# Optimization experiments

Hardware: AMD Instinct MI355X
Metric: run time of the kernel (lower is better)

Reference implementation:

```python
import jax, jax.numpy as jnp
import numpy as np

SEQ = 4096
EMBED = 1280
HEADS = 16
HEAD_DIM = EMBED // HEADS  # 80


def rotate_half(x):
    # interleaved rotate: out[..., 2i] = -x[..., 2i+1]; out[..., 2i+1] = x[..., 2i]
    x_even = x[..., ::2]
    x_odd = x[..., 1::2]
    return jnp.stack((-x_odd, x_even), axis=-1).reshape(x.shape)


def setup_inputs() -> dict:
    key = jax.random.key(0)
    ks = jax.random.split(key, 7)
    return {
        "hidden_states": jax.random.normal(ks[0], (SEQ, EMBED), dtype=jnp.float32),
        "cos": jax.random.uniform(ks[1], (SEQ, HEAD_DIM), dtype=jnp.float32),
        "sin": jax.random.uniform(ks[2], (SEQ, HEAD_DIM), dtype=jnp.float32),
        "w_qkv": jax.random.normal(ks[3], (EMBED, 3 * EMBED), dtype=jnp.float32) * 0.02,
        "b_qkv": jax.random.normal(ks[4], (3 * EMBED,), dtype=jnp.float32) * 0.02,
        "w_proj": jax.random.normal(ks[5], (EMBED, EMBED), dtype=jnp.float32) * 0.02,
        "b_proj": jax.random.normal(ks[6], (EMBED,), dtype=jnp.float32) * 0.02,
    }


def reference(hidden_states, cos, sin, w_qkv, b_qkv, w_proj, b_proj):
    S = hidden_states.shape[0]
    # QKV projection: (S, 3E) -> (S, 3, H, D)
    qkv = (hidden_states @ w_qkv + b_qkv).reshape(S, 3, HEADS, HEAD_DIM)
    q, k, v = qkv[:, 0], qkv[:, 1], qkv[:, 2]  # each (S, H, D)

    # RoPE in float32, cos/sin broadcast over heads: (S, 1, D)
    dt = q.dtype
    qf, kf = q.astype(jnp.float32), k.astype(jnp.float32)
    c = cos[:, None, :].astype(jnp.float32)
    s = sin[:, None, :].astype(jnp.float32)
    q = (qf * c + rotate_half(qf) * s).astype(dt)
    k = (kf * c + rotate_half(kf) * s).astype(dt)

    scaling = HEAD_DIM ** -0.5
    # attention scores per head: (H, S, S)
    scores = jnp.einsum("shd,thd->hst", q, k) * scaling
    attn = jax.nn.softmax(scores.astype(jnp.float32), axis=-1).astype(dt)
    # weighted values: (S, H, D)
    out = jnp.einsum("hst,thd->shd", attn, v).reshape(S, EMBED)
    return out @ w_proj + b_proj
```

## Files before the change

### kernel.cpp

```cpp
#include <hip/hip_runtime.h>
#include <hip/hip_bf16.h>

#define SEQ   4096
#define EMBED 1280
#define NH    16
#define HD    80
#define K1    EMBED
#define N1    (3*EMBED)

typedef short bfrag_t __attribute__((ext_vector_type(8)));
typedef float f32x4   __attribute__((ext_vector_type(4)));
typedef float f32x16  __attribute__((ext_vector_type(16)));

static __device__ __forceinline__ unsigned short f2bf(float x){
    __hip_bfloat16 h = __float2bfloat16(x);
    return __builtin_bit_cast(unsigned short, h);
}
static __device__ __forceinline__ float bf2f(unsigned short u){
    unsigned int v = ((unsigned int)u) << 16;
    return __builtin_bit_cast(float, v);
}

static __device__ __forceinline__ unsigned int pack2bf(float a, float b){
    unsigned int ua = __builtin_bit_cast(unsigned int, a) + 0x8000u;
    unsigned int ub = __builtin_bit_cast(unsigned int, b) + 0x8000u;
#if __has_builtin(__builtin_amdgcn_perm)
    return __builtin_amdgcn_perm(ub, ua, 0x07060302u);
#else
    return (ua >> 16) | (ub & 0xFFFF0000u);
#endif
}

static __device__ __forceinline__ float fast_exp2(float x){
#if __has_builtin(__builtin_amdgcn_exp2f)
    return __builtin_amdgcn_exp2f(x);
#else
    return __expf(x * 0.69314718056f);
#endif
}

static __device__ __forceinline__ void gload_lds16(const void* g, void* l){
#if __has_builtin(__builtin_amdgcn_global_load_lds)
    __builtin_amdgcn_global_load_lds(
        (const __attribute__((address_space(1))) unsigned int*)g,
        (__attribute__((address_space(3))) unsigned int*)l, 16, 0, 0);
#else
    *(uint4*)l = *(const uint4*)g;
#endif
}

static __device__ __forceinline__ bfrag_t ld_frag8(const unsigned short* p){
    uint2 lo = *(const uint2*)p;
    uint2 hi = *(const uint2*)(p + 4);
    uint4 u; u.x = lo.x; u.y = lo.y; u.z = hi.x; u.w = hi.y;
    return __builtin_bit_cast(bfrag_t, u);
}


__global__ __launch_bounds__(256) void f32_to_bf16_k(const float* __restrict__ in,
                                                     unsigned short* __restrict__ out){
    int i = blockIdx.x * 256 + threadIdx.x;
    float4 v = ((const float4*)in)[i];
    ushort4 r;
    r.x = f2bf(v.x); r.y = f2bf(v.y); r.z = f2bf(v.z); r.w = f2bf(v.w);
    ((ushort4*)out)[i] = r;
}

__global__ __launch_bounds__(256) void transpose_to_bf16(const float* __restrict__ in,
                                                         unsigned short* __restrict__ out,
                                                         int R, int C){
    __shared__ float t[32][33];
    int bc = blockIdx.x * 32, br = blockIdx.y * 32;
    int tx = threadIdx.x & 31, ty = threadIdx.x >> 5;
    for (int i = ty; i < 32; i += 8) t[i][tx] = in[(size_t)(br + i) * C + bc + tx];
    __syncthreads();
    for (int i = ty; i < 32; i += 8) out[(size_t)(bc + i) * R + br + tx] = f2bf(t[tx][i]);
}


__global__ __launch_bounds__(256)
void gemm_qkv(const unsigned short* __restrict__ A,
              const unsigned short* __restrict__ BT,
              const float* __restrict__ bias,
              const float* __restrict__ cosp, const float* __restrict__ sinp,
              unsigned short* __restrict__ qout, unsigned short* __restrict__ kout,
              unsigned short* __restrict__ vout,
              int M, int N, int K)
{
    __shared__ union {
        struct { unsigned short A[128*32]; unsigned short B[128*32]; } ab;
        unsigned short tr[4][64][72];
    } lds;

    int tid  = threadIdx.x;
    int lane = tid & 63, wave = tid >> 6;
    int wm = wave >> 1, wn = wave & 1;
    int quad = lane >> 4, l16 = lane & 15;
    int m0 = blockIdx.y * 128, n0 = blockIdx.x * 128;

    f32x4 acc[4][4] = {};
    const unsigned short* ga = A  + (size_t)(m0 + (tid>>2)) * K + (tid&3)*8;
    const unsigned short* gb = BT + (size_t)(n0 + (tid>>2)) * K + (tid&3)*8;

    for (int k0 = 0; k0 < K; k0 += 32){
        __syncthreads();
        gload_lds16(ga,                &lds.ab.A[tid*8]);
        gload_lds16(ga + (size_t)64*K, &lds.ab.A[2048 + tid*8]);
        gload_lds16(gb,                &lds.ab.B[tid*8]);
        gload_lds16(gb + (size_t)64*K, &lds.ab.B[2048 + tid*8]);
        ga += 32; gb += 32;
        __syncthreads();
        bfrag_t af[4], bf[4];
        #pragma unroll
        for (int i = 0; i < 4; i++)
            af[i] = *(const bfrag_t*)&lds.ab.A[(wm*64 + i*16 + l16)*32 + quad*8];
        #pragma unroll
        for (int j = 0; j < 4; j++)
            bf[j] = *(const bfrag_t*)&lds.ab.B[(wn*64 + j*16 + l16)*32 + quad*8];
        #pragma unroll
        for (int i = 0; i < 4; i++)
            #pragma unroll
            for (int j = 0; j < 4; j++)
                acc[i][j] = __builtin_amdgcn_mfma_f32_16x16x32_bf16(af[i], bf[j], acc[i][j], 0, 0, 0);
    }

    const float scaling = 0.11180339887498949f;

    if (n0 >= 2*EMBED){
        __syncthreads();
        #pragma unroll
        for (int j = 0; j < 4; j++){
            int colw = j*16 + l16;
            float b = bias[n0 + wn*64 + colw];
            #pragma unroll
            for (int i = 0; i < 4; i++){
                ushort4 u;
                u.x = f2bf(acc[i][j][0] + b);
                u.y = f2bf(acc[i][j][1] + b);
                u.z = f2bf(acc[i][j][2] + b);
                u.w = f2bf(acc[i][j][3] + b);
                *(ushort4*)&lds.tr[wave][colw][i*16 + quad*4] = u;
            }
        }
        int c8 = lane >> 3, rc = lane & 7;
        #pragma unroll
        for (int cg = 0; cg < 8; cg++){
            int colw = cg*8 + c8;
            size_t colg = (size_t)(n0 - 2*EMBED) + wn*64 + colw;
            int rowg = m0 + wm*64 + rc*8;
            *(uint4*)&vout[colg*SEQ + rowg] = *(const uint4*)&lds.tr[wave][colw][rc*8];
        }
        return;
    }

    #pragma unroll
    for (int i = 0; i < 4; i++)
    #pragma unroll
    for (int j = 0; j < 4; j++){
        int col = n0 + wn*64 + j*16 + l16;
        float b = bias[col];
        #pragma unroll
        for (int r = 0; r < 4; r++){
            int row = m0 + wm*64 + i*16 + quad*4 + r;
            float v = acc[i][j][r] + b;
            int which = col / EMBED;
            int rem   = col % EMBED;
            int h = rem / HD, d = rem % HD;
            float vo = __shfl_xor(v, 1, 64);
            float c = cosp[(size_t)row*HD + d];
            float s = sinp[(size_t)row*HD + d];
            float o = (d & 1) ? (v*c + vo*s) : (v*c - vo*s);
            if (which == 0)
                qout[((size_t)h*SEQ + row)*HD + d] = f2bf(o * scaling);
            else
                kout[((size_t)h*SEQ + row)*HD + d] = f2bf(o);
        }
    }
}


__global__ __launch_bounds__(256)
void gemm_proj(const unsigned short* __restrict__ A,
               const unsigned short* __restrict__ BT,
               const float* __restrict__ bias,
               float* __restrict__ out,
               int M, int N, int K)
{
    __shared__ unsigned short As[64*32];
    __shared__ unsigned short Bs[128*32];
    int tid  = threadIdx.x;
    int lane = tid & 63, wave = tid >> 6;
    int wm = wave & 1, wn = wave >> 1;
    int quad = lane >> 4, l16 = lane & 15;
    int m0 = blockIdx.y * 64, n0 = blockIdx.x * 128;

    f32x4 acc[2][4] = {};
    const unsigned short* ga = A  + (size_t)(m0 + (tid>>2)) * K + (tid&3)*8;
    const unsigned short* gb = BT + (size_t)(n0 + (tid>>2)) * K + (tid&3)*8;

    for (int k0 = 0; k0 < K; k0 += 32){
        __syncthreads();
        gload_lds16(ga,                &As[tid*8]);
        gload_lds16(gb,                &Bs[tid*8]);
        gload_lds16(gb + (size_t)64*K, &Bs[2048 + tid*8]);
        ga += 32; gb += 32;
        __syncthreads();
        bfrag_t af[2], bf[4];
        #pragma unroll
        for (int i = 0; i < 2; i++)
            af[i] = *(const bfrag_t*)&As[(wm*32 + i*16 + l16)*32 + quad*8];
        #pragma unroll
        for (int j = 0; j < 4; j++)
            bf[j] = *(const bfrag_t*)&Bs[(wn*64 + j*16 + l16)*32 + quad*8];
        #pragma unroll
        for (int i = 0; i < 2; i++)
            #pragma unroll
            for (int j = 0; j < 4; j++)
                acc[i][j] = __builtin_amdgcn_mfma_f32_16x16x32_bf16(af[i], bf[j], acc[i][j], 0, 0, 0);
    }

    #pragma unroll
    for (int i = 0; i < 2; i++)
    #pragma unroll
    for (int j = 0; j < 4; j++){
        int col = n0 + wn*64 + j*16 + l16;
        float b = bias[col];
        #pragma unroll
        for (int r = 0; r < 4; r++){
            int row = m0 + wm*32 + i*16 + quad*4 + r;
            out[(size_t)row * N + col] = acc[i][j][r] + b;
        }
    }
}


__global__ __launch_bounds__(256, 4)
void attn_mfma(const unsigned short* __restrict__ q,
               const unsigned short* __restrict__ k,
               const unsigned short* __restrict__ vt,
               unsigned short* __restrict__ out,
               unsigned short* __restrict__ opart,
               float* __restrict__ lpart,
               int iters)
{
    __shared__ unsigned short Vt[2][80*64];
    __shared__ unsigned short Ps[128][68];

    int tid  = threadIdx.x;
    int lane = tid & 63, wave = tid >> 6;
    int quad = lane >> 4, l16 = lane & 15;
    int l32  = lane & 31, h2 = lane >> 5;
    int h = blockIdx.y, q0 = blockIdx.x * 128;
    int split = blockIdx.z;
    int kb0 = split * iters * 64;
    int qrow = wave*32 + l32;

    const unsigned short* qh = q  + ((size_t)h*SEQ + q0)*HD;
    const unsigned short* kh = k  + (size_t)h*SEQ*HD;
    const unsigned short* vh = vt + (size_t)h*HD*SEQ;

    bfrag_t qf[5];
    #pragma unroll
    for (int kk = 0; kk < 5; kk++)
        qf[kk] = *(const bfrag_t*)&qh[(size_t)qrow*HD + (kk*2 + h2)*8];

    auto stage = [&](int buf, int kb){
        unsigned short* dst = &Vt[buf][0];
        #pragma unroll
        for (int rnd = 0; rnd < 3; rnd++){
            int idx = rnd*256 + tid;
            if (rnd < 2 || tid < 128){
                int row = idx >> 3, c = idx & 7;
                gload_lds16(&vh[(size_t)row*SEQ + kb + ((c ^ (row & 7)) << 3)], &dst[idx*8]);
            }
        }
    };

    stage(0, kb0);

    float la = 0.f, lb = 0.f;
    f32x4 o_[2][5] = {};

    const unsigned short* kp = kh + (size_t)(kb0 + l32)*HD + h2*8;
    const float LOG2E = 1.44269504f;
    const float BIAS2 = -17.3123405f;

    for (int kt = 0; kt < iters; kt++){
        f32x16 S0 = {}, S1 = {};
        #pragma unroll
        for (int kk = 0; kk < 5; kk++){
            bfrag_t kf0 = *(const bfrag_t*)(kp + kk*16);
            bfrag_t kf1 = *(const bfrag_t*)(kp + (size_t)32*HD + kk*16);
            S0 = __builtin_amdgcn_mfma_f32_32x32x16_bf16(kf0, qf[kk], S0, 0,0,0);
            S1 = __builtin_amdgcn_mfma_f32_32x32x16_bf16(kf1, qf[kk], S1, 0,0,0);
        }
        kp += (size_t)64*HD;

        #pragma unroll
        for (int r = 0; r < 16; r++){
            float p0 = fast_exp2(fmaf(S0[r], LOG2E, BIAS2));
            float p1 = fast_exp2(fmaf(S1[r], LOG2E, BIAS2));
            S0[r] = p0; S1[r] = p1;
            la += p0; lb += p1;
        }

        #pragma unroll
        for (int g = 0; g < 4; g++){
            uint2 w0, w1;
            w0.x = pack2bf(S0[g*4+0], S0[g*4+1]);
            w0.y = pack2bf(S0[g*4+2], S0[g*4+3]);
            w1.x = pack2bf(S1[g*4+0], S1[g*4+1]);
            w1.y = pack2bf(S1[g*4+2], S1[g*4+3]);
            *(uint2*)&Ps[qrow][g*8 + h2*4]      = w0;
            *(uint2*)&Ps[qrow][32 + g*8 + h2*4] = w1;
        }

        __syncthreads();
        if (kt + 1 < iters) stage((kt+1)&1, kb0 + (kt+1)*64);

        int buf = kt & 1;
        #pragma unroll
        for (int kk = 0; kk < 2; kk++){
            bfrag_t pf0 = ld_frag8(&Ps[wave*32      + l16][kk*32 + quad*8]);
            bfrag_t pf1 = ld_frag8(&Ps[wave*32 + 16 + l16][kk*32 + quad*8]);
            #pragma unroll
            for (int dt = 0; dt < 5; dt++){
                int row = dt*16 + l16;
                bfrag_t vf = *(const bfrag_t*)&Vt[buf][row*64 + (((kk*4+quad) ^ (l16 & 7)) << 3)];
                o_[0][dt] = __builtin_amdgcn_mfma_f32_16x16x32_bf16(vf, pf0, o_[0][dt], 0,0,0);
                o_[1][dt] = __builtin_amdgcn_mfma_f32_16x16x32_bf16(vf, pf1, o_[1][dt], 0,0,0);
            }
        }
    }

    float l_ = la + lb;
    l_ += __shfl_xor(l_, 32, 64);

    if (gridDim.z == 1){
        #pragma unroll
        for (int i = 0; i < 2; i++){
            float linv = 1.f / __shfl(l_, i*16 + l16, 64);
            int qg = q0 + wave*32 + i*16 + l16;
            #pragma unroll
            for (int dt = 0; dt < 5; dt++){
                int d = dt*16 + quad*4;
                ushort4 u;
                u.x = f2bf(o_[i][dt][0]*linv);
                u.y = f2bf(o_[i][dt][1]*linv);
                u.z = f2bf(o_[i][dt][2]*linv);
                u.w = f2bf(o_[i][dt][3]*linv);
                *(ushort4*)&out[(size_t)qg*EMBED + h*HD + d] = u;
            }
        }
    } else {
        if (h2 == 0)
            lpart[((size_t)(split*NH + h))*SEQ + q0 + qrow] = l_;
        #pragma unroll
        for (int i = 0; i < 2; i++){
            int qg = q0 + wave*32 + i*16 + l16;
            size_t base = (((size_t)(split*NH + h))*SEQ + qg)*HD;
            #pragma unroll
            for (int dt = 0; dt < 5; dt++){
                int d = dt*16 + quad*4;
                ushort4 u;
                u.x = f2bf(o_[i][dt][0]);
                u.y = f2bf(o_[i][dt][1]);
                u.z = f2bf(o_[i][dt][2]);
                u.w = f2bf(o_[i][dt][3]);
                *(ushort4*)&opart[base + d] = u;
            }
        }
    }
}

__global__ __launch_bounds__(256)
void attn_combine(const unsigned short* __restrict__ op,
                  const float* __restrict__ lp,
                  unsigned short* __restrict__ out)
{
    int t = blockIdx.x*256 + threadIdx.x;
    int d8 = t % 10;
    int qh = t / 10;
    int q  = qh & (SEQ-1);
    int h  = qh >> 12;
    size_t b0 = (((size_t)h*SEQ) + q)*HD + d8*8;
    size_t b1 = (((size_t)(NH + h)*SEQ) + q)*HD + d8*8;
    float inv = 1.f / (lp[(size_t)h*SEQ + q] + lp[(size_t)(NH + h)*SEQ + q]);
    uint4 A = *(const uint4*)&op[b0];
    uint4 B = *(const uint4*)&op[b1];
    uint4 R;
    unsigned int* a = (unsigned int*)&A;
    unsigned int* b = (unsigned int*)&B;
    unsigned int* r = (unsigned int*)&R;
    #pragma unroll
    for (int e = 0; e < 4; e++){
        float lo = (bf2f((unsigned short)(a[e] & 0xffff)) + bf2f((unsigned short)(b[e] & 0xffff))) * inv;
        float hi = (bf2f((unsigned short)(a[e] >> 16))    + bf2f((unsigned short)(b[e] >> 16)))    * inv;
        r[e] = pack2bf(lo, hi);
    }
    *(uint4*)&out[(size_t)q*EMBED + h*HD + d8*8] = R;
}


extern "C" void kernel_launch(void* const* d_in, const int* in_sizes, int n_in,
                              void* d_out, int out_size, void* d_ws, size_t ws_size,
                              hipStream_t stream)
{
    const float* hs    = (const float*)d_in[0];
    const float* cosp  = (const float*)d_in[1];
    const float* sinp  = (const float*)d_in[2];
    const float* wqkv  = (const float*)d_in[3];
    const float* bqkv  = (const float*)d_in[4];
    const float* wproj = (const float*)d_in[5];
    const float* bproj = (const float*)d_in[6];
    float* out = (float*)d_out;

    char* ws = (char*)d_ws;
    size_t off = 0;
    auto alloc = [&](size_t bytes){ void* p = ws + off; off += bytes; return p; };
    unsigned short* hb    = (unsigned short*)alloc((size_t)SEQ*EMBED*2);
    unsigned short* wqT   = (unsigned short*)alloc((size_t)N1*K1*2);
    unsigned short* wpT   = (unsigned short*)alloc((size_t)EMBED*EMBED*2);
    unsigned short* q_ws  = (unsigned short*)alloc((size_t)SEQ*EMBED*2);
    unsigned short* k_ws  = (unsigned short*)alloc((size_t)SEQ*EMBED*2);
    unsigned short* v_ws  = (unsigned short*)alloc((size_t)SEQ*EMBED*2);
    unsigned short* a_ws  = (unsigned short*)alloc((size_t)SEQ*EMBED*2);
    unsigned short* opart = (unsigned short*)alloc((size_t)2*NH*SEQ*HD*2);
    float*          lpart = (float*)alloc((size_t)2*NH*SEQ*4);
    int nsplit = (ws_size >= off) ? 2 : 1;

    f32_to_bf16_k<<<SEQ*EMBED/4/256, 256, 0, stream>>>(hs, hb);
    transpose_to_bf16<<<dim3(N1/32,    K1/32),    256, 0, stream>>>(wqkv,  wqT, K1,    N1);
    transpose_to_bf16<<<dim3(EMBED/32, EMBED/32), 256, 0, stream>>>(wproj, wpT, EMBED, EMBED);

    gemm_qkv<<<dim3(N1/128, SEQ/128), 256, 0, stream>>>(
        hb, wqT, bqkv, cosp, sinp, q_ws, k_ws, v_ws, SEQ, N1, K1);

    attn_mfma<<<dim3(SEQ/128, NH, nsplit), 256, 0, stream>>>(
        q_ws, k_ws, v_ws, a_ws, opart, lpart, (SEQ/64)/nsplit);
    if (nsplit == 2)
        attn_combine<<<NH*SEQ*10/256, 256, 0, stream>>>(opart, lpart, a_ws);

    gemm_proj<<<dim3(EMBED/128, SEQ/64), 256, 0, stream>>>(
        a_ws, wpT, bproj, out, SEQ, EMBED, EMBED);
}
```

Measured before the change: 330.0 us.

## Merge prep kernels, allow 4-way KV split, simplify QKV epilogue, set occupancy bounds

Folds the hidden-state conversion and both weight transposes into a single launch, removing two kernel launches. The attention KV split can now be 4-way when the workspace allows, with a combine kernel generalized to any split count, which raises grid parallelism at the cost of more partial output traffic. The QKV epilogue hoists the per-column index math and the q/k branch out of the inner loop. Both GEMMs get a launch_bounds minimum of 4 blocks, which may constrain register allocation.

```diff
diff --git a/kernel.cpp b/kernel.cpp
--- a/kernel.cpp
+++ b/kernel.cpp
@@ -56,29 +56,45 @@
     return __builtin_bit_cast(bfrag_t, u);
 }
 
-
-__global__ __launch_bounds__(256) void f32_to_bf16_k(const float* __restrict__ in,
-                                                     unsigned short* __restrict__ out){
-    int i = blockIdx.x * 256 + threadIdx.x;
-    float4 v = ((const float4*)in)[i];
-    ushort4 r;
-    r.x = f2bf(v.x); r.y = f2bf(v.y); r.z = f2bf(v.z); r.w = f2bf(v.w);
-    ((ushort4*)out)[i] = r;
-}
-
-__global__ __launch_bounds__(256) void transpose_to_bf16(const float* __restrict__ in,
-                                                         unsigned short* __restrict__ out,
-                                                         int R, int C){
+#define CONV_BLOCKS (SEQ*EMBED/4/256)
+#define TQ_BX (N1/32)
+#define TQ_BLOCKS (TQ_BX*(K1/32))
+#define TP_BX (EMBED/32)
+#define TP_BLOCKS (TP_BX*(EMBED/32))
+
+__global__ __launch_bounds__(256)
+void prep_all(const float* __restrict__ hs, unsigned short* __restrict__ hb,
+              const float* __restrict__ wqkv, unsigned short* __restrict__ wqT,
+              const float* __restrict__ wproj, unsigned short* __restrict__ wpT)
+{
     __shared__ float t[32][33];
-    int bc = blockIdx.x * 32, br = blockIdx.y * 32;
+    int b = blockIdx.x;
+    if (b < CONV_BLOCKS){
+        int i = b * 256 + threadIdx.x;
+        float4 v = ((const float4*)hs)[i];
+        ushort4 r;
+        r.x = f2bf(v.x); r.y = f2bf(v.y); r.z = f2bf(v.z); r.w = f2bf(v.w);
+        ((ushort4*)hb)[i] = r;
+        return;
+    }
+    const float* in; unsigned short* outp; int R, C, bc, br;
+    if (b < CONV_BLOCKS + TQ_BLOCKS){
+        b -= CONV_BLOCKS;
+        in = wqkv; outp = wqT; R = K1; C = N1;
+        bc = (b % TQ_BX) * 32; br = (b / TQ_BX) * 32;
+    } else {
+        b -= CONV_BLOCKS + TQ_BLOCKS;
+        in = wproj; outp = wpT; R = EMBED; C = EMBED;
+        bc = (b % TP_BX) * 32; br = (b / TP_BX) * 32;
+    }
     int tx = threadIdx.x & 31, ty = threadIdx.x >> 5;
     for (int i = ty; i < 32; i += 8) t[i][tx] = in[(size_t)(br + i) * C + bc + tx];
     __syncthreads();
-    for (int i = ty; i < 32; i += 8) out[(size_t)(bc + i) * R + br + tx] = f2bf(t[tx][i]);
-}
-
-
-__global__ __launch_bounds__(256)
+    for (int i = ty; i < 32; i += 8) outp[(size_t)(bc + i) * R + br + tx] = f2bf(t[tx][i]);
+}
+
+
+__global__ __launch_bounds__(256, 4)
 void gemm_qkv(const unsigned short* __restrict__ A,
               const unsigned short* __restrict__ BT,
               const float* __restrict__ bias,
@@ -157,29 +173,29 @@
     for (int i = 0; i < 4; i++)
     #pragma unroll
     for (int j = 0; j < 4; j++){
-        int col = n0 + wn*64 + j*16 + l16;
-        float b = bias[col];
+        int colj  = n0 + wn*64 + j*16;
+        int which = colj / EMBED;
+        int rem   = colj - which*EMBED;
+        int hh    = rem / HD;
+        int dd    = rem - hh*HD;
+        float b = bias[colj + l16];
+        unsigned short* dst = (which == 0) ? qout : kout;
+        float mult = (which == 0) ? scaling : 1.f;
         #pragma unroll
         for (int r = 0; r < 4; r++){
             int row = m0 + wm*64 + i*16 + quad*4 + r;
             float v = acc[i][j][r] + b;
-            int which = col / EMBED;
-            int rem   = col % EMBED;
-            int h = rem / HD, d = rem % HD;
             float vo = __shfl_xor(v, 1, 64);
-            float c = cosp[(size_t)row*HD + d];
-            float s = sinp[(size_t)row*HD + d];
-            float o = (d & 1) ? (v*c + vo*s) : (v*c - vo*s);
-            if (which == 0)
-                qout[((size_t)h*SEQ + row)*HD + d] = f2bf(o * scaling);
-            else
-                kout[((size_t)h*SEQ + row)*HD + d] = f2bf(o);
-        }
-    }
-}
-
-
-__global__ __launch_bounds__(256)
+            float c = cosp[(size_t)row*HD + dd + l16];
+            float s = sinp[(size_t)row*HD + dd + l16];
+            float o = (l16 & 1) ? (v*c + vo*s) : (v*c - vo*s);
+            dst[((size_t)hh*SEQ + row)*HD + dd + l16] = f2bf(o * mult);
+        }
+    }
+}
+
+
+__global__ __launch_bounds__(256, 4)
 void gemm_proj(const unsigned short* __restrict__ A,
                const unsigned short* __restrict__ BT,
                const float* __restrict__ bias,
@@ -376,28 +392,32 @@
 __global__ __launch_bounds__(256)
 void attn_combine(const unsigned short* __restrict__ op,
                   const float* __restrict__ lp,
-                  unsigned short* __restrict__ out)
+                  unsigned short* __restrict__ out,
+                  int ns)
 {
     int t = blockIdx.x*256 + threadIdx.x;
     int d8 = t % 10;
     int qh = t / 10;
     int q  = qh & (SEQ-1);
     int h  = qh >> 12;
-    size_t b0 = (((size_t)h*SEQ) + q)*HD + d8*8;
-    size_t b1 = (((size_t)(NH + h)*SEQ) + q)*HD + d8*8;
-    float inv = 1.f / (lp[(size_t)h*SEQ + q] + lp[(size_t)(NH + h)*SEQ + q]);
-    uint4 A = *(const uint4*)&op[b0];
-    uint4 B = *(const uint4*)&op[b1];
+    float lsum = 0.f;
+    for (int s = 0; s < ns; s++) lsum += lp[((size_t)(s*NH + h))*SEQ + q];
+    float inv = 1.f / lsum;
+    float acc[8] = {};
+    for (int s = 0; s < ns; s++){
+        uint4 A = *(const uint4*)&op[(((size_t)(s*NH + h))*SEQ + q)*HD + d8*8];
+        unsigned int* a = (unsigned int*)&A;
+        #pragma unroll
+        for (int e = 0; e < 4; e++){
+            acc[2*e]   += bf2f((unsigned short)(a[e] & 0xffff));
+            acc[2*e+1] += bf2f((unsigned short)(a[e] >> 16));
+        }
+    }
     uint4 R;
-    unsigned int* a = (unsigned int*)&A;
-    unsigned int* b = (unsigned int*)&B;
     unsigned int* r = (unsigned int*)&R;
     #pragma unroll
-    for (int e = 0; e < 4; e++){
-        float lo = (bf2f((unsigned short)(a[e] & 0xffff)) + bf2f((unsigned short)(b[e] & 0xffff))) * inv;
-        float hi = (bf2f((unsigned short)(a[e] >> 16))    + bf2f((unsigned short)(b[e] >> 16)))    * inv;
-        r[e] = pack2bf(lo, hi);
-    }
+    for (int e = 0; e < 4; e++)
+        r[e] = pack2bf(acc[2*e]*inv, acc[2*e+1]*inv);
     *(uint4*)&out[(size_t)q*EMBED + h*HD + d8*8] = R;
 }
 
@@ -425,21 +445,24 @@
     unsigned short* k_ws  = (unsigned short*)alloc((size_t)SEQ*EMBED*2);
     unsigned short* v_ws  = (unsigned short*)alloc((size_t)SEQ*EMBED*2);
     unsigned short* a_ws  = (unsigned short*)alloc((size_t)SEQ*EMBED*2);
-    unsigned short* opart = (unsigned short*)alloc((size_t)2*NH*SEQ*HD*2);
-    float*          lpart = (float*)alloc((size_t)2*NH*SEQ*4);
-    int nsplit = (ws_size >= off) ? 2 : 1;
-
-    f32_to_bf16_k<<<SEQ*EMBED/4/256, 256, 0, stream>>>(hs, hb);
-    transpose_to_bf16<<<dim3(N1/32,    K1/32),    256, 0, stream>>>(wqkv,  wqT, K1,    N1);
-    transpose_to_bf16<<<dim3(EMBED/32, EMBED/32), 256, 0, stream>>>(wproj, wpT, EMBED, EMBED);
+    size_t base = off;
+    size_t per_split = (size_t)NH*SEQ*HD*2 + (size_t)NH*SEQ*4;
+    int nsplit = 1;
+    if (ws_size >= base + 4*per_split)      nsplit = 4;
+    else if (ws_size >= base + 2*per_split) nsplit = 2;
+    unsigned short* opart = (unsigned short*)alloc((size_t)nsplit*NH*SEQ*HD*2);
+    float*          lpart = (float*)alloc((size_t)nsplit*NH*SEQ*4);
+
+    prep_all<<<CONV_BLOCKS + TQ_BLOCKS + TP_BLOCKS, 256, 0, stream>>>(
+        hs, hb, wqkv, wqT, wproj, wpT);
 
     gemm_qkv<<<dim3(N1/128, SEQ/128), 256, 0, stream>>>(
         hb, wqT, bqkv, cosp, sinp, q_ws, k_ws, v_ws, SEQ, N1, K1);
 
     attn_mfma<<<dim3(SEQ/128, NH, nsplit), 256, 0, stream>>>(
         q_ws, k_ws, v_ws, a_ws, opart, lpart, (SEQ/64)/nsplit);
-    if (nsplit == 2)
-        attn_combine<<<NH*SEQ*10/256, 256, 0, stream>>>(opart, lpart, a_ws);
+    if (nsplit > 1)
+        attn_combine<<<NH*SEQ*10/256, 256, 0, stream>>>(opart, lpart, a_ws, nsplit);
 
     gemm_proj<<<dim3(EMBED/128, SEQ/64), 256, 0, stream>>>(
         a_ws, wpT, bproj, out, SEQ, EMBED, EMBED);
```

Result: faster. 322.6 us (-2.3%).
